# Kernel optimization log

Measured on AMD Instinct MI355X. Metric: run time of the kernel, lower is better.

## Reference

```python
import jax, jax.numpy as jnp
import numpy as np

# Config mirrors init_kwargs
B, C, K, D = 32768, 100, 8, 512
ROUTING_T = 0.07      # routing_temperature
PRIOR_T = 0.07        # class_prior_temperature
SUB_T = 0.05          # subproto_temperature
RIDGE = 0.1           # ridge (fixed mode)
EPS = 1e-8            # input_norm_eps
PROTO_INIT_SCALE = 0.02


def _l2norm(x, eps=EPS):
    # F.normalize(p=2, dim=-1, eps=eps)
    n = jnp.linalg.norm(x, axis=-1, keepdims=True)
    return x / jnp.maximum(n, eps)


def setup_inputs() -> dict:
    key = jax.random.key(0)
    k1, k2 = jax.random.split(key)
    h = jax.random.normal(k1, (B, D), dtype=jnp.float32)
    # learned parameter: prototypes [num_classes, protos_per_class, feature_dim]
    prototypes = jax.random.normal(k2, (C, K, D), dtype=jnp.float32) * PROTO_INIT_SCALE
    return {"h": h, "prototypes": prototypes}


def reference(h, prototypes):
    # ---- input normalization (input_norm_mode='l2_hypersphere') ----
    hn = _l2norm(h)                                   # [B, D]
    Pn = _l2norm(prototypes)                          # [C, K, D]

    # ---- prototype-distance routing (cosine sims, multiple temperatures) ----
    cos = jnp.einsum('bd,ckd->bck', hn, Pn)           # [B, C, K]
    w_sub = jax.nn.softmax(cos / SUB_T, axis=-1)      # subproto routing weights
    class_sim = jnp.sum(w_sub * cos, axis=-1)         # pooled aggregation [B, C]
    prior_logits = class_sim / PRIOR_T                # class prior logits

    # ---- per-class closed-form ridge solve (same_opp_balanced support) ----
    # Support for class c: its K sub-prototypes (target +1, total weight 0.5)
    # vs. the other C-1 class centers (target -1, total weight 0.5).
    centers = _l2norm(jnp.mean(Pn, axis=1))           # [C, D] pooled class centers
    ws = 0.5 / K
    wo = 0.5 / (C - 1)

    # Gram of same-class support, batched over classes: [C, D, D]
    G_same = ws * jnp.einsum('ckd,cke->cde', Pn, Pn)
    # Opp gram = all-centers gram minus own center outer product
    S_all = centers.T @ centers                       # [D, D]
    G_opp = wo * (S_all[None, :, :] - jnp.einsum('cd,ce->cde', centers, centers))
    A = G_same + G_opp + RIDGE * jnp.eye(D, dtype=h.dtype)  # [C, D, D]

    # RHS X^T S y: +1 on same protos, -1 on opp centers
    b_same = ws * jnp.sum(Pn, axis=1)                 # [C, D]
    csum = jnp.sum(centers, axis=0)                   # [D]
    b_opp = -wo * (csum[None, :] - centers)           # [C, D]
    b = b_same + b_opp

    W = jnp.linalg.solve(A, b[..., None])[..., 0]     # [C, D] per-class ridge weights

    # ---- residual head: routed closed-form logits added to prior ----
    residual = (hn @ W.T) / ROUTING_T                 # [B, C]
    return prior_logits + residual
```

## Files before the change

### kernel.cpp

```cpp
#include <hip/hip_runtime.h>
#include <math.h>

#define NB 32768
#define NC 100
#define NK 8
#define ND 512
#define ALPHA 22.0f
#define NEU_ITERS 12

typedef __attribute__((ext_vector_type(8))) short short8;
typedef __attribute__((ext_vector_type(4))) float f32x4;

__device__ __forceinline__ float warpReduceSum(float v) {
#pragma unroll
    for (int off = 32; off > 0; off >>= 1) v += __shfl_xor(v, off);
    return v;
}

__device__ float blockReduceSum256(float v, float* red) {
    int tid = threadIdx.x;
    v = warpReduceSum(v);
    __syncthreads();
    if ((tid & 63) == 0) red[tid >> 6] = v;
    __syncthreads();
    return red[0] + red[1] + red[2] + red[3];
}

__device__ __forceinline__ unsigned short f2bf(float x) {
    unsigned u = __float_as_uint(x);
    u = (u + 0x7FFFu + ((u >> 16) & 1u)) >> 16;
    return (unsigned short)u;
}
__device__ __forceinline__ float bf2f(unsigned short h) {
    return __uint_as_float(((unsigned)h) << 16);
}


__global__ void k_prep_class(const float* __restrict__ protos, float* __restrict__ X) {
    __shared__ float red[4];
    int c = blockIdx.x;
    int tid = threadIdx.x;
    const float eps = 1e-8f;
    float pv0[NK], pv1[NK];
#pragma unroll
    for (int k = 0; k < NK; ++k) {
        pv0[k] = protos[(c * NK + k) * ND + tid];
        pv1[k] = protos[(c * NK + k) * ND + tid + 256];
    }
    float sv0 = 0.f, sv1 = 0.f;
#pragma unroll
    for (int k = 0; k < NK; ++k) {
        float ss = blockReduceSum256(pv0[k] * pv0[k] + pv1[k] * pv1[k], red);
        float inv = 1.0f / fmaxf(sqrtf(ss), eps);
        pv0[k] *= inv; pv1[k] *= inv;
        X[(c * NK + k) * ND + tid] = pv0[k];
        X[(c * NK + k) * ND + tid + 256] = pv1[k];
        sv0 += pv0[k]; sv1 += pv1[k];
    }
    float ssum = blockReduceSum256(sv0 * sv0 + sv1 * sv1, red);
    float mnorm = sqrtf(ssum) * 0.125f;
    float cinv = 0.125f / fmaxf(mnorm, eps);
    float* centers = X + 800 * ND;
    centers[c * ND + tid] = sv0 * cinv;
    centers[c * ND + tid + 256] = sv1 * cinv;
    const float ws = 0.5f / 8.0f;
    float* bvec = X + 900 * ND;
    bvec[c * ND + tid] = ws * sv0;
    bvec[c * ND + tid + 256] = ws * sv1;
}

__global__ void k_csum(const float* __restrict__ X, float* __restrict__ csum) {
    int d = blockIdx.x * blockDim.x + threadIdx.x;
    const float* centers = X + 800 * ND;
    float s = 0.f;
    for (int c = 0; c < NC; ++c) s += centers[c * ND + d];
    csum[d] = s;
}

__global__ void k_bopp(float* __restrict__ X, const float* __restrict__ csum) {
    int c = blockIdx.x, tid = threadIdx.x;
    const float wo = 0.5f / 99.0f;
    const float* centers = X + 800 * ND;
    float* bvec = X + 900 * ND;
    for (int d = tid; d < ND; d += 256)
        bvec[c * ND + d] -= wo * (csum[d] - centers[c * ND + d]);
}

__global__ void k_gram(const float* __restrict__ X, float* __restrict__ M) {
    __shared__ float cs[ND];
    int i = blockIdx.x, tid = threadIdx.x;
    const float* centers = X + 800 * ND;
    for (int d = tid; d < ND; d += 128) cs[d] = centers[i * ND + d];
    __syncthreads();
    if (tid < NC) {
        const float* cj = centers + tid * ND;
        float s = 0.f;
        for (int d = 0; d < ND; ++d) s += cs[d] * cj[d];
        float ahat = s + ((tid == i) ? (0.1f * 99.0f / 0.5f) : 0.f);
        M[i * NC + tid] = ((tid == i) ? 1.f : 0.f) - ahat * (1.0f / ALPHA);
    }
}

__global__ void k_T1(const float* __restrict__ X, float* __restrict__ T1) {
    __shared__ float xs[ND];
    int j = blockIdx.x, tid = threadIdx.x;
    reinterpret_cast<float4*>(xs)[tid] = reinterpret_cast<const float4*>(X + j * ND)[tid];
    __syncthreads();
    if (tid < NC) {
        const float* ci = X + 800 * ND + tid * ND;
        float s = 0.f;
        for (int d = 0; d < ND; ++d) s += ci[d] * xs[d];
        T1[j * NC + tid] = s;
    }
}

__global__ __launch_bounds__(256) void k_T2neu(const float* __restrict__ M,
                                               const float* __restrict__ T1,
                                               float* __restrict__ T2) {
    __shared__ float Msh[NC * 108];
    __shared__ float pbuf[2][4][104];
    int tid = threadIdx.x;
    int wave = tid >> 6, lane = tid & 63;
    int j = blockIdx.x * 4 + wave;
    for (int idx = tid; idx < NC * NC; idx += 256) {
        int i = idx / NC, m = idx - i * NC;
        Msh[i * 108 + m] = M[idx];
    }
    int i0 = lane;
    int i1 = lane + 64;
    int i1c = (i1 < NC) ? i1 : 0;
    float t0 = T1[j * NC + i0];
    float t1v = (i1 < NC) ? T1[j * NC + i1] : 0.f;
    float s0 = t0, s1 = t1v;
    pbuf[0][wave][i0] = t0;
    if (i1 < NC) pbuf[0][wave][i1] = t1v;
    __syncthreads();
    int cur = 0;
    for (int it = 0; it < NEU_ITERS; ++it) {
        const float* p = pbuf[cur][wave];
        float y0 = 0.f, y1 = 0.f;
#pragma unroll 5
        for (int m = 0; m < NC; m += 4) {
            float4 pv = *reinterpret_cast<const float4*>(p + m);
            float4 a0 = *reinterpret_cast<const float4*>(&Msh[i0 * 108 + m]);
            float4 a1 = *reinterpret_cast<const float4*>(&Msh[i1c * 108 + m]);
            y0 = fmaf(a0.x, pv.x, y0); y0 = fmaf(a0.y, pv.y, y0);
            y0 = fmaf(a0.z, pv.z, y0); y0 = fmaf(a0.w, pv.w, y0);
            y1 = fmaf(a1.x, pv.x, y1); y1 = fmaf(a1.y, pv.y, y1);
            y1 = fmaf(a1.z, pv.z, y1); y1 = fmaf(a1.w, pv.w, y1);
        }
        s0 += y0; s1 += y1;
        int nxt = cur ^ 1;
        pbuf[nxt][wave][i0] = y0;
        if (i1 < NC) pbuf[nxt][wave][i1] = y1;
        cur = nxt;
    }
    T2[j * NC + i0] = s0 * (1.0f / ALPHA);
    if (i1 < NC) T2[j * NC + i1] = s1 * (1.0f / ALPHA);
}

__global__ void k_Y(const float* __restrict__ X, const float* __restrict__ T2,
                    float* __restrict__ Y) {
    __shared__ float t2s[NC];
    int j = blockIdx.x, tid = threadIdx.x;
    for (int i = tid; i < NC; i += 256) t2s[i] = T2[j * NC + i];
    __syncthreads();
    const float* centers = X + 800 * ND;
    for (int d = tid; d < ND; d += 256) {
        float s = 0.f;
        for (int i = 0; i < NC; ++i) s += centers[i * ND + d] * t2s[i];
        Y[j * ND + d] = (X[j * ND + d] - s) * 10.0f;
    }
}

__global__ void k_solve(const float* __restrict__ X, const float* __restrict__ Y,
                        float* __restrict__ W) {
    __shared__ float Vs[9 * 516];
    __shared__ float Ys[10 * 516];
    __shared__ float SL[9 * 10];
    __shared__ float zL[9];
    int c = blockIdx.x, tid = threadIdx.x;
    for (int idx = tid; idx < 9 * 128; idx += 256) {
        int a = idx >> 7, q = idx & 127;
        int row = (a < 8) ? (c * 8 + a) : (800 + c);
        reinterpret_cast<float4*>(&Vs[a * 516])[q] =
            reinterpret_cast<const float4*>(X + row * ND)[q];
    }
    for (int idx = tid; idx < 10 * 128; idx += 256) {
        int a = idx >> 7, q = idx & 127;
        int row = (a < 8) ? (c * 8 + a) : ((a == 8) ? (800 + c) : (900 + c));
        reinterpret_cast<float4*>(&Ys[a * 516])[q] =
            reinterpret_cast<const float4*>(Y + row * ND)[q];
    }
    __syncthreads();
    if (tid < 90) {
        int a = tid / 10, bb = tid - (tid / 10) * 10;
        float s = 0.f;
        for (int d = 0; d < ND; ++d) s += Vs[a * 516 + d] * Ys[bb * 516 + d];
        if (bb == a) s += 16.0f;
        if (bb == a && a == 8) s += -198.0f - 16.0f;
        SL[tid] = s;
    }
    __syncthreads();
    if (tid == 0) {
        for (int p = 0; p < 9; ++p) {
            int best = p; float bv = fabsf(SL[p * 10 + p]);
            for (int r = p + 1; r < 9; ++r) {
                float v = fabsf(SL[r * 10 + p]);
                if (v > bv) { bv = v; best = r; }
            }
            if (best != p)
                for (int j = p; j < 10; ++j) {
                    float t = SL[p * 10 + j]; SL[p * 10 + j] = SL[best * 10 + j]; SL[best * 10 + j] = t;
                }
            float ip = 1.0f / SL[p * 10 + p];
            for (int r = p + 1; r < 9; ++r) {
                float f = SL[r * 10 + p] * ip;
                for (int j = p; j < 10; ++j) SL[r * 10 + j] -= f * SL[p * 10 + j];
            }
        }
        for (int p = 8; p >= 0; --p) {
            float s = SL[p * 10 + 9];
            for (int j = p + 1; j < 9; ++j) s -= SL[p * 10 + j] * zL[j];
            zL[p] = s / SL[p * 10 + p];
        }
    }
    __syncthreads();
    for (int d = tid; d < ND; d += 256) {
        float w = Ys[9 * 516 + d];
#pragma unroll
        for (int a = 0; a < 9; ++a) w -= zL[a] * Ys[a * 516 + d];
        W[c * ND + d] = w;
    }
}


__global__ void k_hn(const float* __restrict__ h, unsigned short* __restrict__ hnb) {
    int tid = threadIdx.x;
    int wave = tid >> 6, lane = tid & 63;
    int r = blockIdx.x * 4 + wave;
    const float4* hp = reinterpret_cast<const float4*>(h + (size_t)r * ND);
    float4 v0 = hp[lane * 2];
    float4 v1 = hp[lane * 2 + 1];
    float s = v0.x * v0.x + v0.y * v0.y + v0.z * v0.z + v0.w * v0.w
            + v1.x * v1.x + v1.y * v1.y + v1.z * v1.z + v1.w * v1.w;
    s = warpReduceSum(s);
    float inv = 1.0f / fmaxf(sqrtf(s), 1e-8f);
    uint4 o;
    o.x = (unsigned)f2bf(v0.x * inv) | ((unsigned)f2bf(v0.y * inv) << 16);
    o.y = (unsigned)f2bf(v0.z * inv) | ((unsigned)f2bf(v0.w * inv) << 16);
    o.z = (unsigned)f2bf(v1.x * inv) | ((unsigned)f2bf(v1.y * inv) << 16);
    o.w = (unsigned)f2bf(v1.z * inv) | ((unsigned)f2bf(v1.w * inv) << 16);
    reinterpret_cast<uint4*>(hnb + (size_t)r * ND)[lane] = o;
}

__global__ void k_packB(const float* __restrict__ X, const float* __restrict__ W,
                        unsigned short* __restrict__ Bp) {
    int tid = threadIdx.x;
    int row = blockIdx.x * 4 + (tid >> 6);
    int lane = tid & 63;
    int c = row / 10, j = row - c * 10;
    float vals[8];
    if (c >= NC) {
#pragma unroll
        for (int q = 0; q < 8; ++q) vals[q] = 0.f;
    } else if (j < 8) {
        const float* src = X + (size_t)(c * 8 + j) * ND + lane * 8;
#pragma unroll
        for (int q = 0; q < 8; ++q) vals[q] = src[q];
    } else {
        const float* src = W + (size_t)c * ND + lane * 8;
#pragma unroll
        for (int q = 0; q < 8; ++q) {
            float w = src[q];
            vals[q] = (j == 8) ? w : (w - bf2f(f2bf(w)));
        }
    }
    uint4 o;
    o.x = (unsigned)f2bf(vals[0]) | ((unsigned)f2bf(vals[1]) << 16);
    o.y = (unsigned)f2bf(vals[2]) | ((unsigned)f2bf(vals[3]) << 16);
    o.z = (unsigned)f2bf(vals[4]) | ((unsigned)f2bf(vals[5]) << 16);
    o.w = (unsigned)f2bf(vals[6]) | ((unsigned)f2bf(vals[7]) << 16);
    reinterpret_cast<uint4*>(Bp + (size_t)row * ND)[lane] = o;
}


__global__ __launch_bounds__(256, 2) void k_main_mfma(
        const unsigned short* __restrict__ hnb, const unsigned short* __restrict__ Bp,
        float* __restrict__ out) {
    __shared__ __align__(16) char smem[41472];
    unsigned short* As = (unsigned short*)smem;
    unsigned short* Bs = (unsigned short*)smem + 9216;
    float* Cs = (float*)smem;

    int tid = threadIdx.x;
    int wave = tid >> 6, lane = tid & 63;
    int m = lane & 15, g = lane >> 4;
    int rowhalf = wave & 1, colhalf = wave >> 1;
    int cb = blockIdx.x;
    int r0 = blockIdx.y * 128;

    f32x4 acc[4][5] = {};

    for (int kc = 0; kc < 8; ++kc) {
        __syncthreads();
        {
            int row = tid >> 1, half = tid & 1;
            const uint4* src = reinterpret_cast<const uint4*>(
                hnb + (size_t)(r0 + row) * ND + kc * 64 + half * 32);
            uint4* dst = reinterpret_cast<uint4*>(As + row * 72 + half * 32);
            dst[0] = src[0]; dst[1] = src[1]; dst[2] = src[2]; dst[3] = src[3];
        }
        for (int idx = tid; idx < 320; idx += 256) {
            int brow = idx >> 1, half = idx & 1;
            int gcol = cb * 160 + brow;
            const uint4* src = reinterpret_cast<const uint4*>(
                Bp + (size_t)gcol * ND + kc * 64 + half * 32);
            uint4* dst = reinterpret_cast<uint4*>(Bs + brow * 72 + half * 32);
            dst[0] = src[0]; dst[1] = src[1]; dst[2] = src[2]; dst[3] = src[3];
        }
        __syncthreads();
#pragma unroll
        for (int kk = 0; kk < 2; ++kk) {
            short8 af[4], bfr[5];
#pragma unroll
            for (int rt = 0; rt < 4; ++rt)
                af[rt] = *reinterpret_cast<const short8*>(
                    As + (rowhalf * 64 + rt * 16 + m) * 72 + kk * 32 + g * 8);
#pragma unroll
            for (int ct = 0; ct < 5; ++ct)
                bfr[ct] = *reinterpret_cast<const short8*>(
                    Bs + (colhalf * 80 + ct * 16 + m) * 72 + kk * 32 + g * 8);
#pragma unroll
            for (int rt = 0; rt < 4; ++rt)
#pragma unroll
                for (int ct = 0; ct < 5; ++ct)
                    acc[rt][ct] = __builtin_amdgcn_mfma_f32_16x16x32_bf16(
                        af[rt], bfr[ct], acc[rt][ct], 0, 0, 0);
        }
    }

    for (int p = 0; p < 2; ++p) {
        __syncthreads();
        if (rowhalf == p) {
#pragma unroll
            for (int rt = 0; rt < 4; ++rt)
#pragma unroll
                for (int ct = 0; ct < 5; ++ct)
#pragma unroll
                    for (int reg = 0; reg < 4; ++reg) {
                        int lr = rt * 16 + g * 4 + reg;
                        int lc = colhalf * 80 + ct * 16 + m;
                        Cs[lr * 162 + lc] = acc[rt][ct][reg];
                    }
        }
        __syncthreads();
        {
            int cl = tid & 15;
            int c = cb * 16 + cl;
#pragma unroll
            for (int q = 0; q < 4; ++q) {
                int r = (tid >> 4) + q * 16;
                float v[10];
#pragma unroll
                for (int j = 0; j < 10; ++j) v[j] = Cs[r * 162 + cl * 10 + j];
                float mx = v[0];
#pragma unroll
                for (int j = 1; j < 8; ++j) mx = fmaxf(mx, v[j]);
                float se = 0.f, sec = 0.f;
#pragma unroll
                for (int j = 0; j < 8; ++j) {
                    float e = __expf((v[j] - mx) * 20.0f);
                    se += e; sec += e * v[j];
                }
                float res = v[8] + v[9];
                if (c < NC)
                    out[(size_t)(r0 + p * 64 + r) * NC + c] =
                        (sec / se + res) * (1.0f / 0.07f);
            }
        }
    }
}

extern "C" void kernel_launch(void* const* d_in, const int* in_sizes, int n_in,
                              void* d_out, int out_size, void* d_ws, size_t ws_size,
                              hipStream_t stream) {
    (void)in_sizes; (void)n_in; (void)out_size; (void)ws_size;
    const float* h = (const float*)d_in[0];
    const float* protos = (const float*)d_in[1];
    float* out = (float*)d_out;
    float* ws = (float*)d_ws;

    float* X    = ws;
    float* csum = X + 512000;
    float* M    = csum + 512;
    float* T1   = M + 10000;
    float* T2   = T1 + 100000;
    float* Y    = T2 + 100000;
    float* W    = Y + 512000;
    unsigned short* hnb = (unsigned short*)(W + 51200);
    unsigned short* Bp  = hnb + (size_t)NB * ND;

    k_hn<<<NB / 4, 256, 0, stream>>>(h, hnb);
    k_prep_class<<<NC, 256, 0, stream>>>(protos, X);
    k_csum<<<2, 256, 0, stream>>>(X, csum);
    k_bopp<<<NC, 256, 0, stream>>>(X, csum);
    k_gram<<<NC, 128, 0, stream>>>(X, M);
    k_T1<<<1000, 128, 0, stream>>>(X, T1);
    k_T2neu<<<250, 256, 0, stream>>>(M, T1, T2);
    k_Y<<<1000, 256, 0, stream>>>(X, T2, Y);
    k_solve<<<NC, 256, 0, stream>>>(X, Y, W);
    k_packB<<<280, 256, 0, stream>>>(X, W, Bp);
    dim3 grid(7, NB / 128);
    k_main_mfma<<<grid, 256, 0, stream>>>(hnb, Bp, out);
}
```

Measured before the change: 275.2 us.

## Use direct global-to-LDS loads with XOR swizzle and transpose centers for coalescing

The main MFMA kernel now stages A and B tiles with global_load_lds (direct global-to-LDS DMA) into an unpadded, XOR-swizzled LDS layout instead of going through registers. Its launch bounds move to 3 blocks per CU and the epilogue stride is padded to 163. A transposed copy of the class centers is written in prep so the gram and T1 kernels read it coalesced across threads rather than strided per thread. The changes aim to cut register pressure and load latency in the main GEMM and uncoalesced accesses in the small kernels, at the cost of an extra workspace buffer and tighter register limits that could cause spills.

```diff
diff --git a/kernel.cpp b/kernel.cpp
--- a/kernel.cpp
+++ b/kernel.cpp
@@ -11,6 +11,12 @@
 typedef __attribute__((ext_vector_type(8))) short short8;
 typedef __attribute__((ext_vector_type(4))) float f32x4;
 
+__device__ __forceinline__ void gl_lds16(const void* g, void* l) {
+    __builtin_amdgcn_global_load_lds(
+        (const __attribute__((address_space(1))) void*)g,
+        (__attribute__((address_space(3))) void*)l, 16, 0, 0);
+}
+
 __device__ __forceinline__ float warpReduceSum(float v) {
 #pragma unroll
     for (int off = 32; off > 0; off >>= 1) v += __shfl_xor(v, off);
@@ -36,7 +42,8 @@
 }
 
 
-__global__ void k_prep_class(const float* __restrict__ protos, float* __restrict__ X) {
+__global__ void k_prep_class(const float* __restrict__ protos, float* __restrict__ X,
+                             float* __restrict__ centersT) {
     __shared__ float red[4];
     int c = blockIdx.x;
     int tid = threadIdx.x;
@@ -61,8 +68,11 @@
     float mnorm = sqrtf(ssum) * 0.125f;
     float cinv = 0.125f / fmaxf(mnorm, eps);
     float* centers = X + 800 * ND;
-    centers[c * ND + tid] = sv0 * cinv;
-    centers[c * ND + tid + 256] = sv1 * cinv;
+    float c0 = sv0 * cinv, c1 = sv1 * cinv;
+    centers[c * ND + tid] = c0;
+    centers[c * ND + tid + 256] = c1;
+    centersT[tid * NC + c] = c0;
+    centersT[(tid + 256) * NC + c] = c1;
     const float ws = 0.5f / 8.0f;
     float* bvec = X + 900 * ND;
     bvec[c * ND + tid] = ws * sv0;
@@ -86,30 +96,32 @@
         bvec[c * ND + d] -= wo * (csum[d] - centers[c * ND + d]);
 }
 
-__global__ void k_gram(const float* __restrict__ X, float* __restrict__ M) {
+__global__ void k_gram(const float* __restrict__ X, const float* __restrict__ centersT,
+                       float* __restrict__ M) {
     __shared__ float cs[ND];
     int i = blockIdx.x, tid = threadIdx.x;
     const float* centers = X + 800 * ND;
     for (int d = tid; d < ND; d += 128) cs[d] = centers[i * ND + d];
     __syncthreads();
     if (tid < NC) {
-        const float* cj = centers + tid * ND;
         float s = 0.f;
-        for (int d = 0; d < ND; ++d) s += cs[d] * cj[d];
+#pragma unroll 8
+        for (int d = 0; d < ND; ++d) s += cs[d] * centersT[d * NC + tid];
         float ahat = s + ((tid == i) ? (0.1f * 99.0f / 0.5f) : 0.f);
         M[i * NC + tid] = ((tid == i) ? 1.f : 0.f) - ahat * (1.0f / ALPHA);
     }
 }
 
-__global__ void k_T1(const float* __restrict__ X, float* __restrict__ T1) {
+__global__ void k_T1(const float* __restrict__ X, const float* __restrict__ centersT,
+                     float* __restrict__ T1) {
     __shared__ float xs[ND];
     int j = blockIdx.x, tid = threadIdx.x;
     reinterpret_cast<float4*>(xs)[tid] = reinterpret_cast<const float4*>(X + j * ND)[tid];
     __syncthreads();
     if (tid < NC) {
-        const float* ci = X + 800 * ND + tid * ND;
         float s = 0.f;
-        for (int d = 0; d < ND; ++d) s += ci[d] * xs[d];
+#pragma unroll 8
+        for (int d = 0; d < ND; ++d) s += xs[d] * centersT[d * NC + tid];
         T1[j * NC + tid] = s;
     }
 }
@@ -285,39 +297,42 @@
 }
 
 
-__global__ __launch_bounds__(256, 2) void k_main_mfma(
+__global__ __launch_bounds__(256, 3) void k_main_mfma(
         const unsigned short* __restrict__ hnb, const unsigned short* __restrict__ Bp,
         float* __restrict__ out) {
-    __shared__ __align__(16) char smem[41472];
+    __shared__ __align__(16) char smem[41728];
     unsigned short* As = (unsigned short*)smem;
-    unsigned short* Bs = (unsigned short*)smem + 9216;
+    unsigned short* Bs = (unsigned short*)smem + 8192;
     float* Cs = (float*)smem;
 
     int tid = threadIdx.x;
     int wave = tid >> 6, lane = tid & 63;
     int m = lane & 15, g = lane >> 4;
+    int rs = m & 7;
     int rowhalf = wave & 1, colhalf = wave >> 1;
     int cb = blockIdx.x;
     int r0 = blockIdx.y * 128;
 
+    int rsub = lane >> 3;
+    int osw = (lane & 7) ^ rsub;
+
     f32x4 acc[4][5] = {};
 
     for (int kc = 0; kc < 8; ++kc) {
         __syncthreads();
-        {
-            int row = tid >> 1, half = tid & 1;
-            const uint4* src = reinterpret_cast<const uint4*>(
-                hnb + (size_t)(r0 + row) * ND + kc * 64 + half * 32);
-            uint4* dst = reinterpret_cast<uint4*>(As + row * 72 + half * 32);
-            dst[0] = src[0]; dst[1] = src[1]; dst[2] = src[2]; dst[3] = src[3];
-        }
-        for (int idx = tid; idx < 320; idx += 256) {
-            int brow = idx >> 1, half = idx & 1;
-            int gcol = cb * 160 + brow;
-            const uint4* src = reinterpret_cast<const uint4*>(
-                Bp + (size_t)gcol * ND + kc * 64 + half * 32);
-            uint4* dst = reinterpret_cast<uint4*>(Bs + brow * 72 + half * 32);
-            dst[0] = src[0]; dst[1] = src[1]; dst[2] = src[2]; dst[3] = src[3];
+#pragma unroll
+        for (int q = 0; q < 4; ++q) {
+            int ch = wave * 4 + q;
+            const unsigned short* gp =
+                hnb + (size_t)(r0 + ch * 8 + rsub) * ND + kc * 64 + osw * 8;
+            gl_lds16(gp, As + ch * 512);
+        }
+#pragma unroll
+        for (int q = 0; q < 5; ++q) {
+            int ch = wave * 5 + q;
+            const unsigned short* gp =
+                Bp + (size_t)(cb * 160 + ch * 8 + rsub) * ND + kc * 64 + osw * 8;
+            gl_lds16(gp, Bs + ch * 512);
         }
         __syncthreads();
 #pragma unroll
@@ -326,11 +341,11 @@
 #pragma unroll
             for (int rt = 0; rt < 4; ++rt)
                 af[rt] = *reinterpret_cast<const short8*>(
-                    As + (rowhalf * 64 + rt * 16 + m) * 72 + kk * 32 + g * 8);
+                    As + (rowhalf * 64 + rt * 16 + m) * 64 + (((kk << 2) + g) ^ rs) * 8);
 #pragma unroll
             for (int ct = 0; ct < 5; ++ct)
                 bfr[ct] = *reinterpret_cast<const short8*>(
-                    Bs + (colhalf * 80 + ct * 16 + m) * 72 + kk * 32 + g * 8);
+                    Bs + (colhalf * 80 + ct * 16 + m) * 64 + (((kk << 2) + g) ^ rs) * 8);
 #pragma unroll
             for (int rt = 0; rt < 4; ++rt)
 #pragma unroll
@@ -351,7 +366,7 @@
                     for (int reg = 0; reg < 4; ++reg) {
                         int lr = rt * 16 + g * 4 + reg;
                         int lc = colhalf * 80 + ct * 16 + m;
-                        Cs[lr * 162 + lc] = acc[rt][ct][reg];
+                        Cs[lr * 163 + lc] = acc[rt][ct][reg];
                     }
         }
         __syncthreads();
@@ -363,7 +378,7 @@
                 int r = (tid >> 4) + q * 16;
                 float v[10];
 #pragma unroll
-                for (int j = 0; j < 10; ++j) v[j] = Cs[r * 162 + cl * 10 + j];
+                for (int j = 0; j < 10; ++j) v[j] = Cs[r * 163 + cl * 10 + j];
                 float mx = v[0];
 #pragma unroll
                 for (int j = 1; j < 8; ++j) mx = fmaxf(mx, v[j]);
@@ -391,22 +406,23 @@
     float* out = (float*)d_out;
     float* ws = (float*)d_ws;
 
-    float* X    = ws;
-    float* csum = X + 512000;
-    float* M    = csum + 512;
-    float* T1   = M + 10000;
-    float* T2   = T1 + 100000;
-    float* Y    = T2 + 100000;
-    float* W    = Y + 512000;
-    unsigned short* hnb = (unsigned short*)(W + 51200);
+    float* X        = ws;
+    float* csum     = X + 512000;
+    float* M        = csum + 512;
+    float* T1       = M + 10000;
+    float* T2       = T1 + 100000;
+    float* Y        = T2 + 100000;
+    float* W        = Y + 512000;
+    float* centersT = W + 51200;
+    unsigned short* hnb = (unsigned short*)(centersT + 51200);
     unsigned short* Bp  = hnb + (size_t)NB * ND;
 
     k_hn<<<NB / 4, 256, 0, stream>>>(h, hnb);
-    k_prep_class<<<NC, 256, 0, stream>>>(protos, X);
+    k_prep_class<<<NC, 256, 0, stream>>>(protos, X, centersT);
     k_csum<<<2, 256, 0, stream>>>(X, csum);
     k_bopp<<<NC, 256, 0, stream>>>(X, csum);
-    k_gram<<<NC, 128, 0, stream>>>(X, M);
-    k_T1<<<1000, 128, 0, stream>>>(X, T1);
+    k_gram<<<NC, 128, 0, stream>>>(X, centersT, M);
+    k_T1<<<1000, 128, 0, stream>>>(X, centersT, T1);
     k_T2neu<<<250, 256, 0, stream>>>(M, T1, T2);
     k_Y<<<1000, 256, 0, stream>>>(X, T2, Y);
     k_solve<<<NC, 256, 0, stream>>>(X, Y, W);
```

Result: no change. 278.7 us (+1.3%).
